# Optimization experiments

Measured on AMD Instinct MI355X. Metric: run time of the kernel, lower is better.

The kernel has to match this reference:

```python
import jax, jax.numpy as jnp
import numpy as np

N, E, D, O, M = 50000, 800000, 128, 128, 2

def _wn(x, v, g, b):
    # weight_norm linear: W = g * v / ||v||_row ; y = x @ W.T + b
    w = g * v / jnp.linalg.norm(v, axis=1, keepdims=True)
    return x @ w.T + b

def _gelu(x):
    return jax.nn.gelu(x, approximate=False)  # torch F.gelu default is exact erf

def setup_inputs() -> dict:
    key = jax.random.key(0)
    ks = jax.random.split(key, 32)
    inp = {"feat": jax.random.normal(ks[0], (N, D), jnp.float32)}
    layers = [("asrc", D, O), ("adst", D, O), ("asub", D, O), ("amul", D, O), ("aout", O, 1),
              ("pool", D, D), ("pool2", D, D), ("self", D, O), ("neigh", D, O), ("neigh2", D, O)]
    for i, (nm, fi, fo) in enumerate(layers):
        inp[nm + "_v"] = jax.random.normal(ks[i + 1], (fo, fi), jnp.float32) * (1.0 / np.sqrt(fi))
        inp[nm + "_g"] = jnp.ones((fo, 1), jnp.float32)
        inp[nm + "_b"] = jnp.zeros((fo,), jnp.float32)
    inp["mlp_v"] = jax.random.normal(ks[20], (M, O, O), jnp.float32) * (1.0 / np.sqrt(O))
    inp["mlp_g"] = jnp.ones((M, O, 1), jnp.float32)
    inp["mlp_b"] = jnp.zeros((M, O), jnp.float32)
    inp["src"] = jax.random.randint(ks[21], (E,), 0, N)
    inp["dst"] = jax.random.randint(ks[22], (E,), 0, N)
    return inp

def reference(feat, asrc_v, asrc_g, asrc_b, adst_v, adst_g, adst_b,
              asub_v, asub_g, asub_b, amul_v, amul_g, amul_b,
              aout_v, aout_g, aout_b, pool_v, pool_g, pool_b,
              pool2_v, pool2_g, pool2_b, self_v, self_g, self_b,
              neigh_v, neigh_g, neigh_b, neigh2_v, neigh2_g, neigh2_b,
              mlp_v, mlp_g, mlp_b, src, dst):
    fs, fd = feat[src], feat[dst]                        # [E, D] gathers
    e = (_wn(fs - fd, asub_v, asub_g, asub_b)
         + _wn(fs * fd, amul_v, amul_g, amul_b)
         + _wn(feat, asrc_v, asrc_g, asrc_b)[src]
         + _wn(feat, adst_v, adst_g, adst_b)[dst])       # [E, O]
    e = _gelu(e)
    e = jax.nn.leaky_relu(_wn(e, aout_v, aout_g, aout_b), 0.2)  # [E, 1] attention scalar

    cnt = jax.ops.segment_sum(jnp.ones((E,), feat.dtype), dst, num_segments=N)[:, None]  # in-degree

    h = _gelu(_wn(feat, pool_v, pool_g, pool_b))         # [N, D]
    neigh = jax.ops.segment_max(e * h[src], dst, num_segments=N)
    neigh = jnp.where(cnt > 0, neigh, jnp.zeros_like(neigh))  # zero for isolated dst nodes

    h2 = _gelu(_wn(feat, pool2_v, pool2_g, pool2_b))
    neigh2 = jax.ops.segment_sum(e * h2[src], dst, num_segments=N) / jnp.maximum(cnt, 1.0)

    rst = (_wn(feat, self_v, self_g, self_b)
           + _wn(neigh, neigh_v, neigh_g, neigh_b)
           + _wn(neigh2, neigh2_v, neigh2_g, neigh2_b))
    for i in range(M):
        rst = rst + _wn(_gelu(rst), mlp_v[i], mlp_g[i], mlp_b[i])
    return rst
```

## Files before the change

kernel.cpp:

```cpp
#include <hip/hip_runtime.h>
#include <hip/hip_bf16.h>
#include <math.h>

constexpr int NN = 50000;
constexpr int EE = 800000;

constexpr int OFF_WT_NODE  = 0;
constexpr int OFF_WT_AMUL  = 65536;
constexpr int OFF_WT_FINAL = 81920;
constexpr int OFF_WT_MLP   = 131072;
constexpr int OFF_WAOUT    = 163840;
constexpr int OFF_BE       = 163968;
constexpr int OFF_BFIN     = 164096;
constexpr int OFF_BAOUT    = 164224;
constexpr int OFF_WNODEBF  = 164240;
constexpr int OFF_WFINBF   = OFF_WNODEBF + 32768;
constexpr int OFF_WMLPBF   = OFF_WFINBF + 24576;
constexpr int OFF_WAMULBF  = OFF_WMLPBF + 16384;
constexpr int OFF_FEATBF   = OFF_WAMULBF + 8192;
constexpr int OFF_SBF      = OFF_FEATBF + NN*64;
constexpr int OFF_WEDGEBF  = OFF_SBF;
constexpr int OFF_HBF      = OFF_SBF + NN*128;
constexpr int OFF_SEV      = OFF_HBF + NN*128;
constexpr int OFF_NEIGHBF  = OFF_SEV + EE;
constexpr int OFF_STARTS   = OFF_NEIGHBF + NN*128;
constexpr int OFF_HIST     = OFF_STARTS + NN + 8;
constexpr int OFF_CURSOR   = OFF_HIST + NN;
constexpr int OFF_SSRCD    = OFF_CURSOR + NN;

constexpr int SCAN_NB = (NN + 255) / 256;

typedef __attribute__((ext_vector_type(8))) short bf16x8;
typedef __attribute__((ext_vector_type(4))) float f32x4;

__device__ __forceinline__ float gelu_f(float x) {
    float x2 = x * x;
    float w = x * fmaf(-0.1029448f, x2, -2.3022082f);
    return x * __builtin_amdgcn_rcpf(1.0f + __builtin_amdgcn_exp2f(w));
}
__device__ __forceinline__ float leaky_f(float x) {
    return x > 0.0f ? x : 0.2f * x;
}
__device__ __forceinline__ unsigned short f2bf(float x) {
    unsigned u = __float_as_uint(x);
    return (unsigned short)((u + 0x7fffu + ((u >> 16) & 1u)) >> 16);
}
__device__ __forceinline__ float bf2f(unsigned short b) {
    return __uint_as_float(((unsigned)b) << 16);
}
__device__ __forceinline__ unsigned pk_bf16(float lo, float hi) {
    __hip_bfloat16 l = __float2bfloat16(lo);
    __hip_bfloat16 h = __float2bfloat16(hi);
    unsigned short lu = *reinterpret_cast<unsigned short*>(&l);
    unsigned short hu = *reinterpret_cast<unsigned short*>(&h);
    return (unsigned)lu | ((unsigned)hu << 16);
}
__device__ __forceinline__ unsigned mulpack(unsigned a, unsigned b) {
    float a0 = __uint_as_float(a << 16), a1 = __uint_as_float(a & 0xffff0000u);
    float b0 = __uint_as_float(b << 16), b1 = __uint_as_float(b & 0xffff0000u);
    return pk_bf16(a0 * b0, a1 * b1);
}
__device__ __forceinline__ float block_sum128(float v, float* sbuf) {
    #pragma unroll
    for (int o = 32; o > 0; o >>= 1) v += __shfl_down(v, o, 64);
    int lane = threadIdx.x & 63, w = threadIdx.x >> 6;
    if (lane == 0) sbuf[w] = v;
    __syncthreads();
    float r = sbuf[0] + sbuf[1];
    __syncthreads();
    return r;
}

struct WnormArgs {
    const float *asrc_v, *asrc_g, *asrc_b;
    const float *adst_v, *adst_g, *adst_b;
    const float *asub_v, *asub_g, *asub_b;
    const float *amul_v, *amul_g, *amul_b;
    const float *aout_v, *aout_g, *aout_b;
    const float *pool_v, *pool_g, *pool_b;
    const float *pool2_v, *pool2_g, *pool2_b;
    const float *self_v, *self_g, *self_b;
    const float *neigh_v, *neigh_g, *neigh_b;
    const float *neigh2_v, *neigh2_g, *neigh2_b;
    const float *mlp_v, *mlp_g, *mlp_b;
    float* ws;
};

__global__ __launch_bounds__(128) void wnorm_kernel(WnormArgs a) {
    __shared__ float sbuf[2];
    int bid = blockIdx.x, i = threadIdx.x;
    float* ws = a.ws;
    if (bid < 1280) {
        int o = bid & 127, grp = bid >> 7;
        const float *v1 = nullptr, *g1 = nullptr, *v2 = nullptr, *g2 = nullptr;
        float sgn2 = 1.0f; float* dst = nullptr; int stride = 0;
        switch (grp) {
            case 0: v1=a.asrc_v; g1=a.asrc_g; v2=a.asub_v; g2=a.asub_g; sgn2= 1.f; dst=ws+OFF_WT_NODE+o;        stride=512; break;
            case 1: v1=a.adst_v; g1=a.adst_g; v2=a.asub_v; g2=a.asub_g; sgn2=-1.f; dst=ws+OFF_WT_NODE+128+o;    stride=512; break;
            case 2: v1=a.pool_v;  g1=a.pool_g;  dst=ws+OFF_WT_NODE+256+o;          stride=512; break;
            case 3: v1=a.pool2_v; g1=a.pool2_g; dst=ws+OFF_WT_NODE+384+o;          stride=512; break;
            case 4: v1=a.amul_v;  g1=a.amul_g;  dst=ws+OFF_WT_AMUL+o;              stride=128; break;
            case 5: v1=a.neigh_v; g1=a.neigh_g; dst=ws+OFF_WT_FINAL+o;             stride=128; break;
            case 6: v1=a.neigh2_v;g1=a.neigh2_g;dst=ws+OFF_WT_FINAL+128*128+o;     stride=128; break;
            case 7: v1=a.self_v;  g1=a.self_g;  dst=ws+OFF_WT_FINAL+256*128+o;     stride=128; break;
            case 8: v1=a.mlp_v;        g1=a.mlp_g;     dst=ws+OFF_WT_MLP+o;        stride=128; break;
            case 9: v1=a.mlp_v+16384;  g1=a.mlp_g+128; dst=ws+OFF_WT_MLP+16384+o;  stride=128; break;
        }
        float x1 = v1[o*128 + i];
        float n1 = sqrtf(block_sum128(x1*x1, sbuf));
        float w = g1[o] * x1 / n1;
        if (v2) {
            float x2 = v2[o*128 + i];
            float n2 = sqrtf(block_sum128(x2*x2, sbuf));
            w += sgn2 * g2[o] * x2 / n2;
        }
        dst[i * stride] = w;
    } else {
        float v = a.aout_v[i];
        float n = sqrtf(block_sum128(v*v, sbuf));
        ws[OFF_WAOUT + i] = a.aout_g[0] * v / n;
        ws[OFF_BE + i]    = a.asrc_b[i] + a.adst_b[i] + a.asub_b[i] + a.amul_b[i];
        ws[OFF_BFIN + i]  = a.self_b[i] + a.neigh_b[i] + a.neigh2_b[i];
        if (i == 0) ws[OFF_BAOUT] = a.aout_b[0];
    }
}

__global__ __launch_bounds__(256) void convert_feat_kernel(const float* __restrict__ feat,
                                                           unsigned short* __restrict__ featbf) {
    int i = (blockIdx.x * 256 + threadIdx.x) * 8;
    float4 v0 = ((const float4*)feat)[i >> 2];
    float4 v1 = ((const float4*)feat)[(i >> 2) + 1];
    uint4 p;
    p.x = pk_bf16(v0.x, v0.y);
    p.y = pk_bf16(v0.z, v0.w);
    p.z = pk_bf16(v1.x, v1.y);
    p.w = pk_bf16(v1.z, v1.w);
    *(uint4*)&featbf[i] = p;
}

__global__ __launch_bounds__(256) void convert_weights_kernel(float* __restrict__ ws) {
    int idx = blockIdx.x * 256 + threadIdx.x;
    unsigned short* wnodebf = (unsigned short*)(ws + OFF_WNODEBF);
    unsigned short* wfinbf  = (unsigned short*)(ws + OFF_WFINBF);
    unsigned short* wmlpbf  = (unsigned short*)(ws + OFF_WMLPBF);
    unsigned short* wamulbf = (unsigned short*)(ws + OFF_WAMULBF);
    unsigned short* wedgebf = (unsigned short*)(ws + OFF_WEDGEBF);
    if (idx < 65536) {
        int k = idx >> 9, n = idx & 511;
        wnodebf[n * 128 + k] = f2bf(ws[OFF_WT_NODE + k * 512 + n]);
    } else if (idx < 114688) {
        int i = idx - 65536, k = i >> 7, o = i & 127;
        wfinbf[o * 384 + k] = f2bf(ws[OFF_WT_FINAL + k * 128 + o]);
    } else if (idx < 147456) {
        int i = idx - 114688, l = i >> 14, j = i & 16383, k = j >> 7, o = j & 127;
        wmlpbf[l * 16384 + o * 128 + k] = f2bf(ws[OFF_WT_MLP + l * 16384 + k * 128 + o]);
    } else if (idx < 163840) {
        int i = idx - 147456, k = i >> 7, o = i & 127;
        wamulbf[o * 128 + k] = f2bf(ws[OFF_WT_AMUL + k * 128 + o]);
    } else {
        int i = idx - 163840;
        int elem = i & 7, f = i >> 3;
        int lane = f & 63, kb = (f >> 6) & 3, ts = f >> 8;
        int t = ts / 3, slice = ts - t * 3;
        int o = t * 16 + (lane & 15);
        int kk = kb * 32 + (lane >> 4) * 8 + elem;
        float v = (slice == 0) ? ws[OFF_WT_AMUL + kk * 128 + o]
                : (slice == 1) ? ws[OFF_WT_NODE + kk * 512 + o]
                               : ws[OFF_WT_NODE + kk * 512 + 128 + o];
        wedgebf[i] = f2bf(v);
    }
}

__global__ __launch_bounds__(256) void hist_zero_kernel(float* __restrict__ ws) {
    int i = blockIdx.x * 256 + threadIdx.x;
    if (i < NN) ((int*)(ws + OFF_HIST))[i] = 0;
}

__global__ __launch_bounds__(256) void hist_kernel(const int* __restrict__ dst, float* __restrict__ ws) {
    int e = blockIdx.x * 256 + threadIdx.x;
    if (e < EE) atomicAdd(&((int*)(ws + OFF_HIST))[dst[e]], 1);
}

__global__ __launch_bounds__(256) void scan_blocks_kernel(float* __restrict__ ws) {
    __shared__ int wsum[4];
    const int* hist = (const int*)(ws + OFF_HIST);
    int* starts = (int*)(ws + OFF_STARTS);
    int* bsum = (int*)(ws + OFF_SEV);
    int bid = blockIdx.x, t = threadIdx.x;
    int idx = bid * 256 + t;
    int lane = t & 63, w = t >> 6;
    int v = (idx < NN) ? hist[idx] : 0;
    int s = v;
    #pragma unroll
    for (int o = 1; o < 64; o <<= 1) {
        int u = __shfl_up(s, o, 64);
        if (lane >= o) s += u;
    }
    if (lane == 63) wsum[w] = s;
    __syncthreads();
    int off = 0;
    for (int i = 0; i < w; ++i) off += wsum[i];
    int incl = s + off;
    if (idx < NN) starts[idx] = incl - v;
    if (t == 255) bsum[bid] = incl;
}

__global__ __launch_bounds__(256) void scan_tops_kernel(float* __restrict__ ws) {
    __shared__ int wsum[4];
    int* bsum = (int*)(ws + OFF_SEV);
    int t = threadIdx.x, lane = t & 63, w = t >> 6;
    int v = (t < SCAN_NB) ? bsum[t] : 0;
    int s = v;
    #pragma unroll
    for (int o = 1; o < 64; o <<= 1) {
        int u = __shfl_up(s, o, 64);
        if (lane >= o) s += u;
    }
    if (lane == 63) wsum[w] = s;
    __syncthreads();
    int off = 0;
    for (int i = 0; i < w; ++i) off += wsum[i];
    if (t < SCAN_NB) bsum[t] = s + off - v;
}

__global__ __launch_bounds__(256) void scan_add_kernel(float* __restrict__ ws) {
    int* starts = (int*)(ws + OFF_STARTS);
    int* cursor = (int*)(ws + OFF_CURSOR);
    const int* bsum = (const int*)(ws + OFF_SEV);
    int bid = blockIdx.x, t = threadIdx.x;
    int idx = bid * 256 + t;
    if (idx < NN) {
        int sv = starts[idx] + bsum[bid];
        starts[idx] = sv;
        cursor[idx] = sv;
    }
    if (idx == 0) starts[NN] = EE;
}

__global__ __launch_bounds__(256) void scatteridx_kernel(const int* __restrict__ src,
                                                         const int* __restrict__ dst,
                                                         float* __restrict__ ws) {
    int e = blockIdx.x * 256 + threadIdx.x;
    if (e >= EE) return;
    int d = dst[e];
    int pos = atomicAdd(&((int*)(ws + OFF_CURSOR))[d], 1);
    ((int2*)(ws + OFF_SSRCD))[pos] = make_int2(src[e], d);
}

__global__ __launch_bounds__(256) void segreduce_kernel(float* __restrict__ ws) {
    int n = blockIdx.x * 4 + (threadIdx.x >> 6);
    int lane = threadIdx.x & 63;
    const int* starts = (const int*)(ws + OFF_STARTS);
    const int2* ssrcd = (const int2*)(ws + OFF_SSRCD);
    const float* sev = ws + OFF_SEV;
    const unsigned short* hbf = (const unsigned short*)(ws + OFF_HBF);
    unsigned short* neighbf = (unsigned short*)(ws + OFF_NEIGHBF);
    int s0 = starts[n], s1 = starts[n + 1];
    float2 mx = make_float2(-INFINITY, -INFINITY);
    float2 sm = make_float2(0.f, 0.f);
    int i = s0;
    for (; i + 2 <= s1; i += 2) {
        int sA = ssrcd[i].x, sB = ssrcd[i + 1].x;
        float evA = sev[i], evB = sev[i + 1];
        unsigned hvA  = *(const unsigned*)&hbf[sA * 256 + lane * 2];
        unsigned h2vA = *(const unsigned*)&hbf[sA * 256 + 128 + lane * 2];
        unsigned hvB  = *(const unsigned*)&hbf[sB * 256 + lane * 2];
        unsigned h2vB = *(const unsigned*)&hbf[sB * 256 + 128 + lane * 2];
        mx.x = fmaxf(mx.x, evA * bf2f((unsigned short)(hvA & 0xffffu)));
        mx.y = fmaxf(mx.y, evA * bf2f((unsigned short)(hvA >> 16)));
        sm.x += evA * bf2f((unsigned short)(h2vA & 0xffffu));
        sm.y += evA * bf2f((unsigned short)(h2vA >> 16));
        mx.x = fmaxf(mx.x, evB * bf2f((unsigned short)(hvB & 0xffffu)));
        mx.y = fmaxf(mx.y, evB * bf2f((unsigned short)(hvB >> 16)));
        sm.x += evB * bf2f((unsigned short)(h2vB & 0xffffu));
        sm.y += evB * bf2f((unsigned short)(h2vB >> 16));
    }
    if (i < s1) {
        int s = ssrcd[i].x;
        float ev = sev[i];
        unsigned hv  = *(const unsigned*)&hbf[s * 256 + lane * 2];
        unsigned h2v = *(const unsigned*)&hbf[s * 256 + 128 + lane * 2];
        mx.x = fmaxf(mx.x, ev * bf2f((unsigned short)(hv & 0xffffu)));
        mx.y = fmaxf(mx.y, ev * bf2f((unsigned short)(hv >> 16)));
        sm.x += ev * bf2f((unsigned short)(h2v & 0xffffu));
        sm.y += ev * bf2f((unsigned short)(h2v >> 16));
    }
    int cnt = s1 - s0;
    if (cnt == 0) { mx.x = 0.f; mx.y = 0.f; }
    float ic = 1.0f / (float)max(cnt, 1);
    *(unsigned*)&neighbf[n * 256 + lane * 2] = pk_bf16(mx.x, mx.y);
    *(unsigned*)&neighbf[n * 256 + 128 + lane * 2] = pk_bf16(sm.x * ic, sm.y * ic);
}

__global__ __launch_bounds__(256) void gemm_node_mfma(const unsigned short* __restrict__ featbf,
                                                      const float* __restrict__ pool_b,
                                                      const float* __restrict__ pool2_b,
                                                      unsigned short* __restrict__ hbf,
                                                      const unsigned short* __restrict__ wnodebf) {
    __shared__ unsigned short As[64 * 136];
    int tid = threadIdx.x;
    int row0 = blockIdx.x * 64, gy = blockIdx.y;
    #pragma unroll
    for (int it = 0; it < 4; ++it) {
        int idx = tid + it * 256;
        int r = idx >> 4, u = idx & 15;
        int rr = min(row0 + r, NN - 1);
        *(uint4*)&As[r * 136 + u * 8] = *(const uint4*)&featbf[rr * 128 + u * 8];
    }
    __syncthreads();
    int lane = tid & 63, w = tid >> 6;
    int quad = lane >> 4, l15 = lane & 15;
    const unsigned short* B = wnodebf + (gy + 2) * 128 * 128;
    const float* bias = gy == 0 ? pool_b : pool2_b;
    f32x4 acc[8] = {};
    #pragma unroll 1
    for (int ks = 0; ks < 4; ++ks) {
        bf16x8 a = *(const bf16x8*)&As[(w * 16 + l15) * 136 + ks * 32 + quad * 8];
        #pragma unroll
        for (int t = 0; t < 8; ++t) {
            bf16x8 b = *(const bf16x8*)&B[(t * 16 + l15) * 128 + ks * 32 + quad * 8];
            acc[t] = __builtin_amdgcn_mfma_f32_16x16x32_bf16(a, b, acc[t], 0, 0, 0);
        }
    }
    #pragma unroll
    for (int reg = 0; reg < 4; ++reg) {
        int row = row0 + w * 16 + quad * 4 + reg;
        if (row >= NN) continue;
        #pragma unroll
        for (int t = 0; t < 8; ++t) {
            int col = t * 16 + l15;
            hbf[row * 256 + gy * 128 + col] = f2bf(gelu_f(acc[t][reg] + bias[col]));
        }
    }
}

__global__ __launch_bounds__(256, 3) void gemm_edge(const unsigned short* __restrict__ featbf,
                                                    const unsigned short* __restrict__ wedgebf,
                                                    float* __restrict__ ws) {
    __shared__ unsigned short Bs[2][24 * 512];
    int tid = threadIdx.x;
    int lane = tid & 63, w = tid >> 6;
    int quad = lane >> 4, l15 = lane & 15;
    int e0 = blockIdx.x * 128;
    const int2* ssrcd = (const int2*)(ws + OFF_SSRCD);
    int base = e0 + w * 32 + l15;
    int2 i0 = ssrcd[base];
    int2 i1 = ssrcd[base + 16];
    const unsigned short* p0s = &featbf[i0.x * 128];
    const unsigned short* p0d = &featbf[i0.y * 128];
    const unsigned short* p1s = &featbf[i1.x * 128];
    const unsigned short* p1d = &featbf[i1.y * 128];
    int ko = quad * 8;

    uint4 ca[2][4];
    ca[0][0] = *(const uint4*)&p0s[ko];
    ca[0][1] = *(const uint4*)&p0d[ko];
    ca[0][2] = *(const uint4*)&p1s[ko];
    ca[0][3] = *(const uint4*)&p1d[ko];
    ca[1][0] = *(const uint4*)&p0s[ko + 32];
    ca[1][1] = *(const uint4*)&p0d[ko + 32];
    ca[1][2] = *(const uint4*)&p1s[ko + 32];
    ca[1][3] = *(const uint4*)&p1d[ko + 32];
    uint4 sb[6];
    #pragma unroll
    for (int i = 0; i < 6; ++i) {
        int ts = w * 6 + i;
        sb[i] = *(const uint4*)&wedgebf[(ts * 4 + 0) * 512 + lane * 8];
    }
    #pragma unroll
    for (int i = 0; i < 6; ++i) {
        int ts = w * 6 + i;
        *(uint4*)&Bs[0][ts * 512 + lane * 8] = sb[i];
    }
    __syncthreads();

    f32x4 acc0[8] = {}, acc1[8] = {};
    #pragma unroll
    for (int kb = 0; kb < 4; ++kb) {
        uint4 c0s = ca[kb & 1][0], c0d = ca[kb & 1][1];
        uint4 c1s = ca[kb & 1][2], c1d = ca[kb & 1][3];
        uint4 m0, m1;
        m0.x = mulpack(c0s.x, c0d.x); m0.y = mulpack(c0s.y, c0d.y);
        m0.z = mulpack(c0s.z, c0d.z); m0.w = mulpack(c0s.w, c0d.w);
        m1.x = mulpack(c1s.x, c1d.x); m1.y = mulpack(c1s.y, c1d.y);
        m1.z = mulpack(c1s.z, c1d.z); m1.w = mulpack(c1s.w, c1d.w);
        bf16x8 am0 = *(const bf16x8*)&m0,  am1 = *(const bf16x8*)&m1;
        bf16x8 as0 = *(const bf16x8*)&c0s, ad0 = *(const bf16x8*)&c0d;
        bf16x8 as1 = *(const bf16x8*)&c1s, ad1 = *(const bf16x8*)&c1d;
        if (kb < 2) {
            int k2 = ko + (kb + 2) * 32;
            ca[kb & 1][0] = *(const uint4*)&p0s[k2];
            ca[kb & 1][1] = *(const uint4*)&p0d[k2];
            ca[kb & 1][2] = *(const uint4*)&p1s[k2];
            ca[kb & 1][3] = *(const uint4*)&p1d[k2];
        }
        if (kb < 3) {
            #pragma unroll
            for (int i = 0; i < 6; ++i) {
                int ts = w * 6 + i;
                sb[i] = *(const uint4*)&wedgebf[(ts * 4 + kb + 1) * 512 + lane * 8];
            }
        }
        const unsigned short* bb = &Bs[kb & 1][lane * 8];
        #pragma unroll
        for (int t = 0; t < 8; ++t) {
            bf16x8 bm = *(const bf16x8*)&bb[(t * 3 + 0) * 512];
            bf16x8 b1 = *(const bf16x8*)&bb[(t * 3 + 1) * 512];
            bf16x8 b2 = *(const bf16x8*)&bb[(t * 3 + 2) * 512];
            acc0[t] = __builtin_amdgcn_mfma_f32_16x16x32_bf16(am0, bm, acc0[t], 0, 0, 0);
            acc1[t] = __builtin_amdgcn_mfma_f32_16x16x32_bf16(am1, bm, acc1[t], 0, 0, 0);
            acc0[t] = __builtin_amdgcn_mfma_f32_16x16x32_bf16(as0, b1, acc0[t], 0, 0, 0);
            acc1[t] = __builtin_amdgcn_mfma_f32_16x16x32_bf16(as1, b1, acc1[t], 0, 0, 0);
            acc0[t] = __builtin_amdgcn_mfma_f32_16x16x32_bf16(ad0, b2, acc0[t], 0, 0, 0);
            acc1[t] = __builtin_amdgcn_mfma_f32_16x16x32_bf16(ad1, b2, acc1[t], 0, 0, 0);
        }
        if (kb < 3) {
            #pragma unroll
            for (int i = 0; i < 6; ++i) {
                int ts = w * 6 + i;
                *(uint4*)&Bs[(kb + 1) & 1][ts * 512 + lane * 8] = sb[i];
            }
            __syncthreads();
        }
    }

    const float* waout = ws + OFF_WAOUT;
    const float* be = ws + OFF_BE;
    float b_aout = ws[OFF_BAOUT];
    float* e_out = ws + OFF_SEV;
    float wv[8], bv[8];
    #pragma unroll
    for (int t = 0; t < 8; ++t) { wv[t] = waout[t * 16 + l15]; bv[t] = be[t * 16 + l15]; }
    #pragma unroll
    for (int g = 0; g < 2; ++g) {
        #pragma unroll
        for (int reg = 0; reg < 4; ++reg) {
            int r = w * 32 + g * 16 + quad * 4 + reg;
            float partial = 0.0f;
            #pragma unroll
            for (int t = 0; t < 8; ++t) {
                float v = (g ? acc1[t][reg] : acc0[t][reg]) + bv[t];
                partial += gelu_f(v) * wv[t];
            }
            partial += __shfl_xor(partial, 1, 16);
            partial += __shfl_xor(partial, 2, 16);
            partial += __shfl_xor(partial, 4, 16);
            partial += __shfl_xor(partial, 8, 16);
            if (l15 == 0) e_out[e0 + r] = leaky_f(partial + b_aout);
        }
    }
}

__global__ __launch_bounds__(256) void gemm_final_mfma(const unsigned short* __restrict__ neighbf,
                                                       const unsigned short* __restrict__ featbf,
                                                       const unsigned short* __restrict__ wfinbf,
                                                       float* __restrict__ out,
                                                       const float* __restrict__ ws) {
    __shared__ unsigned short As[64 * 392];
    __shared__ float bfin_s[128];
    int tid = threadIdx.x;
    int row0 = blockIdx.x * 64;
    if (tid < 128) bfin_s[tid] = ws[OFF_BFIN + tid];
    #pragma unroll
    for (int rg = 0; rg < 3; ++rg) {
        #pragma unroll
        for (int it = 0; it < 4; ++it) {
            int idx = tid + it * 256;
            int r = idx >> 4, u = idx & 15;
            int rr = min(row0 + r, NN - 1);
            const unsigned short* sp = (rg == 0) ? &neighbf[rr * 256 + u * 8]
                                     : (rg == 1) ? &neighbf[rr * 256 + 128 + u * 8]
                                                 : &featbf[rr * 128 + u * 8];
            *(uint4*)&As[r * 392 + rg * 128 + u * 8] = *(const uint4*)sp;
        }
    }
    __syncthreads();
    int lane = tid & 63, w = tid >> 6;
    int quad = lane >> 4, l15 = lane & 15;
    f32x4 acc[8] = {};
    #pragma unroll 1
    for (int ks = 0; ks < 12; ++ks) {
        bf16x8 a = *(const bf16x8*)&As[(w * 16 + l15) * 392 + ks * 32 + quad * 8];
        #pragma unroll
        for (int t = 0; t < 8; ++t) {
            bf16x8 b = *(const bf16x8*)&wfinbf[(t * 16 + l15) * 384 + ks * 32 + quad * 8];
            acc[t] = __builtin_amdgcn_mfma_f32_16x16x32_bf16(a, b, acc[t], 0, 0, 0);
        }
    }
    #pragma unroll
    for (int reg = 0; reg < 4; ++reg) {
        int row = row0 + w * 16 + quad * 4 + reg;
        if (row >= NN) continue;
        #pragma unroll
        for (int t = 0; t < 8; ++t) {
            int col = t * 16 + l15;
            out[row * 128 + col] = acc[t][reg] + bfin_s[col];
        }
    }
}

__global__ __launch_bounds__(256) void gemm_mlp_mfma(float* __restrict__ out,
                                                     const unsigned short* __restrict__ wmlp,
                                                     const float* __restrict__ bias) {
    __shared__ unsigned short As[64 * 136];
    int tid = threadIdx.x;
    int row0 = blockIdx.x * 64;
    #pragma unroll
    for (int it = 0; it < 8; ++it) {
        int idx = tid + it * 256;
        int r = idx >> 5, u = idx & 31;
        int rr = min(row0 + r, NN - 1);
        float4 v = ((const float4*)out)[rr * 32 + u];
        unsigned p0 = pk_bf16(gelu_f(v.x), gelu_f(v.y));
        unsigned p1 = pk_bf16(gelu_f(v.z), gelu_f(v.w));
        *(unsigned*)&As[r * 136 + u * 4]     = p0;
        *(unsigned*)&As[r * 136 + u * 4 + 2] = p1;
    }
    __syncthreads();
    int lane = tid & 63, w = tid >> 6;
    int quad = lane >> 4, l15 = lane & 15;
    f32x4 acc[8] = {};
    #pragma unroll 1
    for (int ks = 0; ks < 4; ++ks) {
        bf16x8 a = *(const bf16x8*)&As[(w * 16 + l15) * 136 + ks * 32 + quad * 8];
        #pragma unroll
        for (int t = 0; t < 8; ++t) {
            bf16x8 b = *(const bf16x8*)&wmlp[(t * 16 + l15) * 128 + ks * 32 + quad * 8];
            acc[t] = __builtin_amdgcn_mfma_f32_16x16x32_bf16(a, b, acc[t], 0, 0, 0);
        }
    }
    #pragma unroll
    for (int reg = 0; reg < 4; ++reg) {
        int row = row0 + w * 16 + quad * 4 + reg;
        if (row >= NN) continue;
        #pragma unroll
        for (int t = 0; t < 8; ++t) {
            int col = t * 16 + l15;
            out[row * 128 + col] += acc[t][reg] + bias[col];
        }
    }
}

extern "C" void kernel_launch(void* const* d_in, const int* in_sizes, int n_in,
                              void* d_out, int out_size, void* d_ws, size_t ws_size,
                              hipStream_t stream) {
    const float* feat = (const float*)d_in[0];
    WnormArgs wa;
    wa.asrc_v = (const float*)d_in[1];  wa.asrc_g = (const float*)d_in[2];  wa.asrc_b = (const float*)d_in[3];
    wa.adst_v = (const float*)d_in[4];  wa.adst_g = (const float*)d_in[5];  wa.adst_b = (const float*)d_in[6];
    wa.asub_v = (const float*)d_in[7];  wa.asub_g = (const float*)d_in[8];  wa.asub_b = (const float*)d_in[9];
    wa.amul_v = (const float*)d_in[10]; wa.amul_g = (const float*)d_in[11]; wa.amul_b = (const float*)d_in[12];
    wa.aout_v = (const float*)d_in[13]; wa.aout_g = (const float*)d_in[14]; wa.aout_b = (const float*)d_in[15];
    wa.pool_v = (const float*)d_in[16]; wa.pool_g = (const float*)d_in[17]; wa.pool_b = (const float*)d_in[18];
    wa.pool2_v= (const float*)d_in[19]; wa.pool2_g= (const float*)d_in[20]; wa.pool2_b= (const float*)d_in[21];
    wa.self_v = (const float*)d_in[22]; wa.self_g = (const float*)d_in[23]; wa.self_b = (const float*)d_in[24];
    wa.neigh_v= (const float*)d_in[25]; wa.neigh_g= (const float*)d_in[26]; wa.neigh_b= (const float*)d_in[27];
    wa.neigh2_v=(const float*)d_in[28]; wa.neigh2_g=(const float*)d_in[29]; wa.neigh2_b=(const float*)d_in[30];
    wa.mlp_v  = (const float*)d_in[31]; wa.mlp_g  = (const float*)d_in[32]; wa.mlp_b  = (const float*)d_in[33];
    const int* src = (const int*)d_in[34];
    const int* dst = (const int*)d_in[35];
    float* out = (float*)d_out;
    float* ws = (float*)d_ws;
    wa.ws = ws;
    unsigned short* featbf  = (unsigned short*)(ws + OFF_FEATBF);
    unsigned short* hbf     = (unsigned short*)(ws + OFF_HBF);
    unsigned short* neighbf = (unsigned short*)(ws + OFF_NEIGHBF);
    unsigned short* wnodebf = (unsigned short*)(ws + OFF_WNODEBF);
    unsigned short* wfinbf  = (unsigned short*)(ws + OFF_WFINBF);
    unsigned short* wmlpbf  = (unsigned short*)(ws + OFF_WMLPBF);
    unsigned short* wedgebf = (unsigned short*)(ws + OFF_WEDGEBF);

    wnorm_kernel<<<dim3(1281), dim3(128), 0, stream>>>(wa);
    convert_feat_kernel<<<dim3(NN * 128 / (256 * 8)), dim3(256), 0, stream>>>(feat, featbf);
    convert_weights_kernel<<<dim3(832), dim3(256), 0, stream>>>(ws);
    hist_zero_kernel<<<dim3((NN + 255) / 256), dim3(256), 0, stream>>>(ws);
    hist_kernel<<<dim3((EE + 255) / 256), dim3(256), 0, stream>>>(dst, ws);
    scan_blocks_kernel<<<dim3(SCAN_NB), dim3(256), 0, stream>>>(ws);
    scan_tops_kernel<<<dim3(1), dim3(256), 0, stream>>>(ws);
    scan_add_kernel<<<dim3(SCAN_NB), dim3(256), 0, stream>>>(ws);
    scatteridx_kernel<<<dim3((EE + 255) / 256), dim3(256), 0, stream>>>(src, dst, ws);
    gemm_node_mfma<<<dim3(782, 2), dim3(256), 0, stream>>>(featbf, wa.pool_b, wa.pool2_b, hbf, wnodebf);
    gemm_edge<<<dim3(EE / 128), dim3(256), 0, stream>>>(featbf, wedgebf, ws);
    segreduce_kernel<<<dim3(NN / 4), dim3(256), 0, stream>>>(ws);
    gemm_final_mfma<<<dim3(782), dim3(256), 0, stream>>>(neighbf, featbf, wfinbf, out, ws);
    gemm_mlp_mfma<<<dim3(782), dim3(256), 0, stream>>>(out, wmlpbf, wa.mlp_b);
    gemm_mlp_mfma<<<dim3(782), dim3(256), 0, stream>>>(out, wmlpbf + 16384, wa.mlp_b + 128);
}
```

Before: 531.9 us.

## Fuse feat conversion into node GEMM and MLP layers into final GEMM

Removes the standalone feat-to-bf16 conversion kernel: the node GEMM now reads fp32 feat, converts it into shared memory, writes the bf16 copy for later kernels, and computes both pool and pool2 outputs in one block instead of a 2-wide grid. The final GEMM now keeps the result in registers and applies both residual MLP layers in-kernel via shared memory, which removes two launches and two fp32 round trips of the output. The segment reduction unrolls by 4 to keep more gathers in flight. Costs are higher register pressure in the fused kernels, fewer blocks for the node GEMM, and the node GEMM's column-gy passes now running serially within each block.

Result: faster. 510.3 us (-4.1%).

```diff
diff --git a/kernel.cpp b/kernel.cpp
--- a/kernel.cpp
+++ b/kernel.cpp
@@ -123,19 +123,6 @@
         ws[OFF_BFIN + i]  = a.self_b[i] + a.neigh_b[i] + a.neigh2_b[i];
         if (i == 0) ws[OFF_BAOUT] = a.aout_b[0];
     }
-}
-
-__global__ __launch_bounds__(256) void convert_feat_kernel(const float* __restrict__ feat,
-                                                           unsigned short* __restrict__ featbf) {
-    int i = (blockIdx.x * 256 + threadIdx.x) * 8;
-    float4 v0 = ((const float4*)feat)[i >> 2];
-    float4 v1 = ((const float4*)feat)[(i >> 2) + 1];
-    uint4 p;
-    p.x = pk_bf16(v0.x, v0.y);
-    p.y = pk_bf16(v0.z, v0.w);
-    p.z = pk_bf16(v1.x, v1.y);
-    p.w = pk_bf16(v1.z, v1.w);
-    *(uint4*)&featbf[i] = p;
 }
 
 __global__ __launch_bounds__(256) void convert_weights_kernel(float* __restrict__ ws) {
@@ -259,23 +246,35 @@
     float2 mx = make_float2(-INFINITY, -INFINITY);
     float2 sm = make_float2(0.f, 0.f);
     int i = s0;
-    for (; i + 2 <= s1; i += 2) {
-        int sA = ssrcd[i].x, sB = ssrcd[i + 1].x;
-        float evA = sev[i], evB = sev[i + 1];
-        unsigned hvA  = *(const unsigned*)&hbf[sA * 256 + lane * 2];
-        unsigned h2vA = *(const unsigned*)&hbf[sA * 256 + 128 + lane * 2];
-        unsigned hvB  = *(const unsigned*)&hbf[sB * 256 + lane * 2];
-        unsigned h2vB = *(const unsigned*)&hbf[sB * 256 + 128 + lane * 2];
-        mx.x = fmaxf(mx.x, evA * bf2f((unsigned short)(hvA & 0xffffu)));
-        mx.y = fmaxf(mx.y, evA * bf2f((unsigned short)(hvA >> 16)));
-        sm.x += evA * bf2f((unsigned short)(h2vA & 0xffffu));
-        sm.y += evA * bf2f((unsigned short)(h2vA >> 16));
-        mx.x = fmaxf(mx.x, evB * bf2f((unsigned short)(hvB & 0xffffu)));
-        mx.y = fmaxf(mx.y, evB * bf2f((unsigned short)(hvB >> 16)));
-        sm.x += evB * bf2f((unsigned short)(h2vB & 0xffffu));
-        sm.y += evB * bf2f((unsigned short)(h2vB >> 16));
-    }
-    if (i < s1) {
+    for (; i + 4 <= s1; i += 4) {
+        int sA = ssrcd[i].x, sB = ssrcd[i + 1].x, sC = ssrcd[i + 2].x, sD = ssrcd[i + 3].x;
+        float eA = sev[i], eB = sev[i + 1], eC = sev[i + 2], eD = sev[i + 3];
+        unsigned hA = *(const unsigned*)&hbf[sA * 256 + lane * 2];
+        unsigned gA = *(const unsigned*)&hbf[sA * 256 + 128 + lane * 2];
+        unsigned hB = *(const unsigned*)&hbf[sB * 256 + lane * 2];
+        unsigned gB = *(const unsigned*)&hbf[sB * 256 + 128 + lane * 2];
+        unsigned hC = *(const unsigned*)&hbf[sC * 256 + lane * 2];
+        unsigned gC = *(const unsigned*)&hbf[sC * 256 + 128 + lane * 2];
+        unsigned hD = *(const unsigned*)&hbf[sD * 256 + lane * 2];
+        unsigned gD = *(const unsigned*)&hbf[sD * 256 + 128 + lane * 2];
+        mx.x = fmaxf(mx.x, eA * bf2f((unsigned short)(hA & 0xffffu)));
+        mx.y = fmaxf(mx.y, eA * bf2f((unsigned short)(hA >> 16)));
+        sm.x += eA * bf2f((unsigned short)(gA & 0xffffu));
+        sm.y += eA * bf2f((unsigned short)(gA >> 16));
+        mx.x = fmaxf(mx.x, eB * bf2f((unsigned short)(hB & 0xffffu)));
+        mx.y = fmaxf(mx.y, eB * bf2f((unsigned short)(hB >> 16)));
+        sm.x += eB * bf2f((unsigned short)(gB & 0xffffu));
+        sm.y += eB * bf2f((unsigned short)(gB >> 16));
+        mx.x = fmaxf(mx.x, eC * bf2f((unsigned short)(hC & 0xffffu)));
+        mx.y = fmaxf(mx.y, eC * bf2f((unsigned short)(hC >> 16)));
+        sm.x += eC * bf2f((unsigned short)(gC & 0xffffu));
+        sm.y += eC * bf2f((unsigned short)(gC >> 16));
+        mx.x = fmaxf(mx.x, eD * bf2f((unsigned short)(hD & 0xffffu)));
+        mx.y = fmaxf(mx.y, eD * bf2f((unsigned short)(hD >> 16)));
+        sm.x += eD * bf2f((unsigned short)(gD & 0xffffu));
+        sm.y += eD * bf2f((unsigned short)(gD >> 16));
+    }
+    for (; i < s1; ++i) {
         int s = ssrcd[i].x;
         float ev = sev[i];
         unsigned hv  = *(const unsigned*)&hbf[s * 256 + lane * 2];
@@ -292,44 +291,53 @@
     *(unsigned*)&neighbf[n * 256 + 128 + lane * 2] = pk_bf16(sm.x * ic, sm.y * ic);
 }
 
-__global__ __launch_bounds__(256) void gemm_node_mfma(const unsigned short* __restrict__ featbf,
+__global__ __launch_bounds__(256) void gemm_node_mfma(const float* __restrict__ feat,
                                                       const float* __restrict__ pool_b,
                                                       const float* __restrict__ pool2_b,
+                                                      unsigned short* __restrict__ featbf,
                                                       unsigned short* __restrict__ hbf,
                                                       const unsigned short* __restrict__ wnodebf) {
     __shared__ unsigned short As[64 * 136];
     int tid = threadIdx.x;
-    int row0 = blockIdx.x * 64, gy = blockIdx.y;
-    #pragma unroll
-    for (int it = 0; it < 4; ++it) {
+    int row0 = blockIdx.x * 64;
+    #pragma unroll
+    for (int it = 0; it < 8; ++it) {
         int idx = tid + it * 256;
-        int r = idx >> 4, u = idx & 15;
+        int r = idx >> 5, u = idx & 31;
         int rr = min(row0 + r, NN - 1);
-        *(uint4*)&As[r * 136 + u * 8] = *(const uint4*)&featbf[rr * 128 + u * 8];
+        float4 v = ((const float4*)feat)[rr * 32 + u];
+        unsigned p0 = pk_bf16(v.x, v.y);
+        unsigned p1 = pk_bf16(v.z, v.w);
+        *(unsigned*)&As[r * 136 + u * 4]     = p0;
+        *(unsigned*)&As[r * 136 + u * 4 + 2] = p1;
+        *(uint2*)&featbf[rr * 128 + u * 4] = make_uint2(p0, p1);
     }
     __syncthreads();
     int lane = tid & 63, w = tid >> 6;
     int quad = lane >> 4, l15 = lane & 15;
-    const unsigned short* B = wnodebf + (gy + 2) * 128 * 128;
-    const float* bias = gy == 0 ? pool_b : pool2_b;
-    f32x4 acc[8] = {};
     #pragma unroll 1
-    for (int ks = 0; ks < 4; ++ks) {
-        bf16x8 a = *(const bf16x8*)&As[(w * 16 + l15) * 136 + ks * 32 + quad * 8];
-        #pragma unroll
-        for (int t = 0; t < 8; ++t) {
-            bf16x8 b = *(const bf16x8*)&B[(t * 16 + l15) * 128 + ks * 32 + quad * 8];
-            acc[t] = __builtin_amdgcn_mfma_f32_16x16x32_bf16(a, b, acc[t], 0, 0, 0);
-        }
-    }
-    #pragma unroll
-    for (int reg = 0; reg < 4; ++reg) {
-        int row = row0 + w * 16 + quad * 4 + reg;
-        if (row >= NN) continue;
-        #pragma unroll
-        for (int t = 0; t < 8; ++t) {
-            int col = t * 16 + l15;
-            hbf[row * 256 + gy * 128 + col] = f2bf(gelu_f(acc[t][reg] + bias[col]));
+    for (int gy = 0; gy < 2; ++gy) {
+        const unsigned short* B = wnodebf + (gy + 2) * 128 * 128;
+        const float* bias = gy == 0 ? pool_b : pool2_b;
+        f32x4 acc[8] = {};
+        #pragma unroll 1
+        for (int ks = 0; ks < 4; ++ks) {
+            bf16x8 a = *(const bf16x8*)&As[(w * 16 + l15) * 136 + ks * 32 + quad * 8];
+            #pragma unroll
+            for (int t = 0; t < 8; ++t) {
+                bf16x8 b = *(const bf16x8*)&B[(t * 16 + l15) * 128 + ks * 32 + quad * 8];
+                acc[t] = __builtin_amdgcn_mfma_f32_16x16x32_bf16(a, b, acc[t], 0, 0, 0);
+            }
+        }
+        #pragma unroll
+        for (int reg = 0; reg < 4; ++reg) {
+            int row = row0 + w * 16 + quad * 4 + reg;
+            if (row >= NN) continue;
+            #pragma unroll
+            for (int t = 0; t < 8; ++t) {
+                int col = t * 16 + l15;
+                hbf[row * 256 + gy * 128 + col] = f2bf(gelu_f(acc[t][reg] + bias[col]));
+            }
         }
     }
 }
@@ -451,11 +459,13 @@
     }
 }
 
-__global__ __launch_bounds__(256) void gemm_final_mfma(const unsigned short* __restrict__ neighbf,
-                                                       const unsigned short* __restrict__ featbf,
-                                                       const unsigned short* __restrict__ wfinbf,
-                                                       float* __restrict__ out,
-                                                       const float* __restrict__ ws) {
+__global__ __launch_bounds__(256) void gemm_final_mlp(const unsigned short* __restrict__ neighbf,
+                                                      const unsigned short* __restrict__ featbf,
+                                                      const unsigned short* __restrict__ wfinbf,
+                                                      const unsigned short* __restrict__ wmlpbf,
+                                                      const float* __restrict__ mlp_b,
+                                                      float* __restrict__ out,
+                                                      const float* __restrict__ ws) {
     __shared__ unsigned short As[64 * 392];
     __shared__ float bfin_s[128];
     int tid = threadIdx.x;
@@ -477,14 +487,50 @@
     __syncthreads();
     int lane = tid & 63, w = tid >> 6;
     int quad = lane >> 4, l15 = lane & 15;
-    f32x4 acc[8] = {};
+    f32x4 rst[8] = {};
     #pragma unroll 1
     for (int ks = 0; ks < 12; ++ks) {
         bf16x8 a = *(const bf16x8*)&As[(w * 16 + l15) * 392 + ks * 32 + quad * 8];
         #pragma unroll
         for (int t = 0; t < 8; ++t) {
             bf16x8 b = *(const bf16x8*)&wfinbf[(t * 16 + l15) * 384 + ks * 32 + quad * 8];
-            acc[t] = __builtin_amdgcn_mfma_f32_16x16x32_bf16(a, b, acc[t], 0, 0, 0);
+            rst[t] = __builtin_amdgcn_mfma_f32_16x16x32_bf16(a, b, rst[t], 0, 0, 0);
+        }
+    }
+    #pragma unroll
+    for (int t = 0; t < 8; ++t) {
+        float bf = bfin_s[t * 16 + l15];
+        #pragma unroll
+        for (int reg = 0; reg < 4; ++reg) rst[t][reg] += bf;
+    }
+    #pragma unroll 1
+    for (int layer = 0; layer < 2; ++layer) {
+        __syncthreads();
+        #pragma unroll
+        for (int t = 0; t < 8; ++t) {
+            #pragma unroll
+            for (int reg = 0; reg < 4; ++reg) {
+                int row = w * 16 + quad * 4 + reg;
+                As[row * 136 + t * 16 + l15] = f2bf(gelu_f(rst[t][reg]));
+            }
+        }
+        __syncthreads();
+        const unsigned short* wB = wmlpbf + layer * 16384;
+        f32x4 acc[8] = {};
+        #pragma unroll 1
+        for (int ks = 0; ks < 4; ++ks) {
+            bf16x8 a = *(const bf16x8*)&As[(w * 16 + l15) * 136 + ks * 32 + quad * 8];
+            #pragma unroll
+            for (int t = 0; t < 8; ++t) {
+                bf16x8 b = *(const bf16x8*)&wB[(t * 16 + l15) * 128 + ks * 32 + quad * 8];
+                acc[t] = __builtin_amdgcn_mfma_f32_16x16x32_bf16(a, b, acc[t], 0, 0, 0);
+            }
+        }
+        #pragma unroll
+        for (int t = 0; t < 8; ++t) {
+            float bias = mlp_b[layer * 128 + t * 16 + l15];
+            #pragma unroll
+            for (int reg = 0; reg < 4; ++reg) rst[t][reg] += acc[t][reg] + bias;
         }
     }
     #pragma unroll
@@ -493,50 +539,7 @@
         if (row >= NN) continue;
         #pragma unroll
         for (int t = 0; t < 8; ++t) {
-            int col = t * 16 + l15;
-            out[row * 128 + col] = acc[t][reg] + bfin_s[col];
-        }
-    }
-}
-
-__global__ __launch_bounds__(256) void gemm_mlp_mfma(float* __restrict__ out,
-                                                     const unsigned short* __restrict__ wmlp,
-                                                     const float* __restrict__ bias) {
-    __shared__ unsigned short As[64 * 136];
-    int tid = threadIdx.x;
-    int row0 = blockIdx.x * 64;
-    #pragma unroll
-    for (int it = 0; it < 8; ++it) {
-        int idx = tid + it * 256;
-        int r = idx >> 5, u = idx & 31;
-        int rr = min(row0 + r, NN - 1);
-        float4 v = ((const float4*)out)[rr * 32 + u];
-        unsigned p0 = pk_bf16(gelu_f(v.x), gelu_f(v.y));
-        unsigned p1 = pk_bf16(gelu_f(v.z), gelu_f(v.w));
-        *(unsigned*)&As[r * 136 + u * 4]     = p0;
-        *(unsigned*)&As[r * 136 + u * 4 + 2] = p1;
-    }
-    __syncthreads();
-    int lane = tid & 63, w = tid >> 6;
-    int quad = lane >> 4, l15 = lane & 15;
-    f32x4 acc[8] = {};
-    #pragma unroll 1
-    for (int ks = 0; ks < 4; ++ks) {
-        bf16x8 a = *(const bf16x8*)&As[(w * 16 + l15) * 136 + ks * 32 + quad * 8];
-        #pragma unroll
-        for (int t = 0; t < 8; ++t) {
-            bf16x8 b = *(const bf16x8*)&wmlp[(t * 16 + l15) * 128 + ks * 32 + quad * 8];
-            acc[t] = __builtin_amdgcn_mfma_f32_16x16x32_bf16(a, b, acc[t], 0, 0, 0);
-        }
-    }
-    #pragma unroll
-    for (int reg = 0; reg < 4; ++reg) {
-        int row = row0 + w * 16 + quad * 4 + reg;
-        if (row >= NN) continue;
-        #pragma unroll
-        for (int t = 0; t < 8; ++t) {
-            int col = t * 16 + l15;
-            out[row * 128 + col] += acc[t][reg] + bias[col];
+            out[row * 128 + t * 16 + l15] = rst[t][reg];
         }
     }
 }
@@ -571,7 +574,6 @@
     unsigned short* wedgebf = (unsigned short*)(ws + OFF_WEDGEBF);
 
     wnorm_kernel<<<dim3(1281), dim3(128), 0, stream>>>(wa);
-    convert_feat_kernel<<<dim3(NN * 128 / (256 * 8)), dim3(256), 0, stream>>>(feat, featbf);
     convert_weights_kernel<<<dim3(832), dim3(256), 0, stream>>>(ws);
     hist_zero_kernel<<<dim3((NN + 255) / 256), dim3(256), 0, stream>>>(ws);
     hist_kernel<<<dim3((EE + 255) / 256), dim3(256), 0, stream>>>(dst, ws);
@@ -579,10 +581,8 @@
     scan_tops_kernel<<<dim3(1), dim3(256), 0, stream>>>(ws);
     scan_add_kernel<<<dim3(SCAN_NB), dim3(256), 0, stream>>>(ws);
     scatteridx_kernel<<<dim3((EE + 255) / 256), dim3(256), 0, stream>>>(src, dst, ws);
-    gemm_node_mfma<<<dim3(782, 2), dim3(256), 0, stream>>>(featbf, wa.pool_b, wa.pool2_b, hbf, wnodebf);
+    gemm_node_mfma<<<dim3(782), dim3(256), 0, stream>>>(feat, wa.pool_b, wa.pool2_b, featbf, hbf, wnodebf);
     gemm_edge<<<dim3(EE / 128), dim3(256), 0, stream>>>(featbf, wedgebf, ws);
     segreduce_kernel<<<dim3(NN / 4), dim3(256), 0, stream>>>(ws);
-    gemm_final_mfma<<<dim3(782), dim3(256), 0, stream>>>(neighbf, featbf, wfinbf, out, ws);
-    gemm_mlp_mfma<<<dim3(782), dim3(256), 0, stream>>>(out, wmlpbf, wa.mlp_b);
-    gemm_mlp_mfma<<<dim3(782), dim3(256), 0, stream>>>(out, wmlpbf + 16384, wa.mlp_b + 128);
-}
+    gemm_final_mlp<<<dim3(782), dim3(256), 0, stream>>>(neighbf, featbf, wfinbf, wmlpbf, wa.mlp_b, out, ws);
+}
```
